# Kernel optimization log

Hardware: AMD Instinct MI355X
Metric: run time of the kernel (lower is better)

Reference implementation:

```python
import jax, jax.numpy as jnp
from jax import lax
import numpy as np

EPS = 1e-5

def _bn(x, g, b, m, v):
    # inference-mode BatchNorm2d over channel dim (NCHW)
    scale = (g * lax.rsqrt(v + EPS))[None, :, None, None]
    return (x - m[None, :, None, None]) * scale + b[None, :, None, None]

def _conv(x, w, dil, pad):
    return lax.conv_general_dilated(
        x, w, window_strides=(1, 1), padding=[(pad, pad), (pad, pad)],
        rhs_dilation=(dil, dil), dimension_numbers=('NCHW', 'OIHW', 'NCHW'))

def _interleave(b0, b1, b2, b3):
    # out[2i+r, 2j+c] = branch[2r+c][i, j]  (equivalent to the mask*nearest-upsample trick)
    bs, C, H, W = b0.shape
    row0 = jnp.stack([b0, b1], axis=-1)          # (bs,C,H,W,2) -> c
    row1 = jnp.stack([b2, b3], axis=-1)
    s = jnp.stack([row0, row1], axis=-2)          # (bs,C,H,W,2,2) -> (...,r,c)
    return s.transpose(0, 1, 2, 4, 3, 5).reshape(bs, C, 2 * H, 2 * W)

def setup_inputs() -> dict:
    key = jax.random.key(0)
    ks = iter(jax.random.split(key, 40))
    B, Cin, Cout, H = 8, 256, 128, 64
    inp = {"x": jax.random.normal(next(ks), (B, Cin, H, H), jnp.float32)}
    inp["w0"] = jax.random.normal(next(ks), (Cout, Cin, 1, 1), jnp.float32) * 0.05
    for i in (1, 2, 3):
        inp[f"w{i}"] = jax.random.normal(next(ks), (Cout, Cin, 3, 3), jnp.float32) * 0.02
    inp["wp"] = jax.random.normal(next(ks), (Cout, Cout, 1, 1), jnp.float32) * 0.05
    for t in ("0", "1", "2", "3", "p"):
        inp[f"g{t}"] = 1.0 + 0.1 * jax.random.normal(next(ks), (Cout,), jnp.float32)
        inp[f"b{t}"] = 0.1 * jax.random.normal(next(ks), (Cout,), jnp.float32)
        inp[f"m{t}"] = 0.05 * jax.random.normal(next(ks), (Cout,), jnp.float32)
        inp[f"v{t}"] = jax.random.uniform(next(ks), (Cout,), jnp.float32, 0.5, 1.5)
    return inp

def reference(x, w0, w1, w2, w3, wp,
              g0, b0, m0, v0, g1, b1, m1, v1,
              g2, b2, m2, v2, g3, b3, m3, v3,
              gp, bp, mp, vp):
    RATES = (6, 12, 18)
    br0 = jax.nn.relu(_bn(_conv(x, w0, 1, 0), g0, b0, m0, v0))
    br1 = jax.nn.relu(_bn(_conv(x, w1, RATES[0], RATES[0]), g1, b1, m1, v1))
    br2 = jax.nn.relu(_bn(_conv(x, w2, RATES[1], RATES[1]), g2, b2, m2, v2))
    br3 = jax.nn.relu(_bn(_conv(x, w3, RATES[2], RATES[2]), g3, b3, m3, v3))
    up = _interleave(br0, br1, br2, br3)          # (B, Cout, 2H, 2W)
    return jax.nn.relu(_bn(_conv(up, wp, 1, 0), gp, bp, mp, vp))  # dropout: eval identity
```

## Files before the change

### kernel.cpp

```cpp
#include <hip/hip_runtime.h>
#include <stdint.h>

typedef unsigned int uint32;
typedef uint16_t u16;
typedef short short8 __attribute__((ext_vector_type(8)));
typedef short shortx4 __attribute__((ext_vector_type(4)));
typedef float floatx4 __attribute__((ext_vector_type(4)));

#define BN_EPS 1e-5f

#define XROW 25600
#define XPLANE 1638400
#define XB_SHORTS 13107200
#define ZROW_SHORTS 25600

#define OFF0 0
#define OFF1 32768
#define OFF2 327680
#define OFF3 622592
#define OFFP 917504
#define WPK_SHORTS 933888
#define U_B0 4096
#define U_B  36864
#define U_TOT 116736

__device__ __forceinline__ u16 f2bf(float f) {
  uint32 u = __float_as_uint(f);
  u += 0x7fffu + ((u >> 16) & 1u);
  return (u16)(u >> 16);
}

__global__ void k_xcvt(const float* __restrict__ x, u16* __restrict__ xb) {
  int bid = blockIdx.x, tid = threadIdx.x;
  if (bid == 512) {
    uint32* z = (uint32*)(xb + XB_SHORTS);
    #pragma unroll
    for (int r = 0; r < 50; ++r) z[r * 256 + tid] = 0;
    return;
  }
  int n = bid >> 6, i = bid & 63;
  uint32* rw = (uint32*)(xb + (size_t)n * XPLANE + (size_t)i * XROW);
  #pragma unroll
  for (int e = 0; e < 18; ++e) {
    int idx = e * 256 + tid;
    int colid = idx >> 7;
    int jp = (colid < 18) ? colid : (colid + 64);
    rw[jp * 128 + (idx & 127)] = 0;
  }
  int ci2 = tid & 127, jh = tid >> 7;
  const float* xs = x + ((size_t)(n * 256 + 2 * ci2) * 64 + i) * 64 + jh * 32;
  #pragma unroll 4
  for (int j = 0; j < 32; ++j) {
    float f0 = xs[j];
    float f1 = xs[4096 + j];
    uint32 pk = (uint32)f2bf(f0) | ((uint32)f2bf(f1) << 16);
    rw[(jh * 32 + j + 18) * 128 + ci2] = pk;
  }
}

__global__ void k_wpack(const float* __restrict__ w0, const float* __restrict__ w1,
                        const float* __restrict__ w2, const float* __restrict__ w3,
                        const float* __restrict__ wp, u16* __restrict__ wpk) {
  int g = blockIdx.x * 256 + threadIdx.x;
  if (g >= U_TOT) return;
  const float* w; int Cin, t, q, u, off; bool k3;
  if (g < U_B0) {
    int blk = g >> 10; w = w0; Cin = 256; k3 = false; t = 0; q = blk; u = g & 1023;
    off = OFF0 + blk * 8192;
  } else if (g < U_B0 + U_B) {
    int g1 = g - U_B0; int blk = g1 >> 10; w = w1; Cin = 256; k3 = true;
    t = blk >> 2; q = blk & 3; u = g1 & 1023; off = OFF1 + blk * 8192;
  } else if (g < U_B0 + 2*U_B) {
    int g1 = g - (U_B0 + U_B); int blk = g1 >> 10; w = w2; Cin = 256; k3 = true;
    t = blk >> 2; q = blk & 3; u = g1 & 1023; off = OFF2 + blk * 8192;
  } else if (g < U_B0 + 3*U_B) {
    int g1 = g - (U_B0 + 2*U_B); int blk = g1 >> 10; w = w3; Cin = 256; k3 = true;
    t = blk >> 2; q = blk & 3; u = g1 & 1023; off = OFF3 + blk * 8192;
  } else {
    int g1 = g - (U_B0 + 3*U_B); int blk = g1 >> 10; w = wp; Cin = 128; k3 = false;
    t = 0; q = blk; u = g1 & 1023; off = OFFP + blk * 8192;
  }
  int slot = u >> 7, co = u & 127;
  int ci0 = q * 64 + slot * 8;
  int kh = k3 ? (t / 3) : 0, kw = k3 ? (t % 3) : 0;
  union { short8 s; u16 us[8]; } v;
  #pragma unroll
  for (int e = 0; e < 8; ++e) {
    int ci = ci0 + e;
    float wv = k3 ? w[((co * Cin + ci) * 3 + kh) * 3 + kw] : w[co * Cin + ci];
    v.us[e] = f2bf(wv);
  }
  *(short8*)(wpk + off + u * 8) = v.s;
}

__global__ void k_bn(const float* g0,const float* b0,const float* m0,const float* v0,
                     const float* g1,const float* b1,const float* m1,const float* v1,
                     const float* g2,const float* b2,const float* m2,const float* v2,
                     const float* g3,const float* b3,const float* m3,const float* v3,
                     const float* gp,const float* bp,const float* mp,const float* vp,
                     float* __restrict__ bn) {
  int i = blockIdx.x * 256 + threadIdx.x;
  if (i >= 640) return;
  int t = i >> 7, co = i & 127;
  const float *G, *B, *M, *V;
  if      (t == 0) { G=g0; B=b0; M=m0; V=v0; }
  else if (t == 1) { G=g1; B=b1; M=m1; V=v1; }
  else if (t == 2) { G=g2; B=b2; M=m2; V=v2; }
  else if (t == 3) { G=g3; B=b3; M=m3; V=v3; }
  else             { G=gp; B=bp; M=mp; V=vp; }
  float s = G[co] * rsqrtf(V[co] + BN_EPS);
  bn[t * 256 + co]       = s;
  bn[t * 256 + 128 + co] = B[co] - M[co] * s;
}

__global__ __launch_bounds__(256, 3)
void k_main(const u16* __restrict__ xb, const u16* __restrict__ wpk,
            const float* __restrict__ bn, float* __restrict__ out) {
  __shared__ __align__(16) u16 BP[16384];

  int tid = threadIdx.x;
  int bid = blockIdx.x;
  int n = bid & 7;
  int rest = bid >> 3;
  int tile = rest >> 2;
  int b = (rest ^ (rest >> 5)) & 3;
  int i0 = tile * 2;
  int lane = tid & 63, wid = tid >> 6;
  int wm = wid >> 1, wn = wid & 1;
  int m16 = lane & 15, hh = lane >> 4;

  const u16* xg = xb + (size_t)n * XPLANE;
  const u16* zr = xb + XB_SHORTS;
  int d = (b == 0) ? 0 : ((b == 1) ? 6 : ((b == 2) ? 12 : 18));
  int NS = ((b == 0) ? 1 : 9) * 4;
  int woff8 = ((b == 0) ? OFF0 : (b == 1) ? OFF1 : (b == 2) ? OFF2 : OFF3) / 8;

  const short8* wpk8 = (const short8*)wpk;
  const short8* PsS8 = (const short8*)BP;

  floatx4 acc[4][4];
  #pragma unroll
  for (int a1 = 0; a1 < 4; ++a1)
    #pragma unroll
    for (int a2 = 0; a2 < 4; ++a2) acc[a1][a2] = (floatx4){0.f, 0.f, 0.f, 0.f};

  short8 rb[4];
  int cg = tid & 7, pxo = tid >> 3;
  int arow = wm * 64 + m16;

  auto prefetchB = [&](int s) {
    int t = s >> 2, q = s & 3;
    int di = d * (t / 3 - 1);
    int dj = d * (t % 3 - 1);
    #pragma unroll
    for (int k = 0; k < 4; ++k) {
      int px = k * 32 + pxo;
      int ii = i0 + (k >> 1) + di;
      const u16* base = (ii >= 0 && ii < 64) ? (xg + ii * XROW) : zr;
      int jj = (px & 63) + 18 + dj;
      rb[k] = *(const short8*)(base + jj * 256 + q * 64 + cg * 8);
    }
  };

  prefetchB(0);

  for (int s = 0; s < NS; ++s) {
    short8* Bcur = (short8*)(BP + (s & 1) * 8192);
    #pragma unroll
    for (int k = 0; k < 4; ++k) {
      int px = k * 32 + pxo;
      Bcur[px * 8 + (cg ^ (px & 7))] = rb[k];
    }
    short8 af[2][4];
    {
      int abase = woff8 + s * 1024;
      #pragma unroll
      for (int kk = 0; kk < 2; ++kk)
        #pragma unroll
        for (int f = 0; f < 4; ++f)
          af[kk][f] = wpk8[abase + (kk * 4 + hh) * 128 + arow + f * 16];
    }
    if (s + 1 < NS) prefetchB(s + 1);
    asm volatile("s_waitcnt lgkmcnt(0)" ::: "memory");
    __builtin_amdgcn_s_barrier();
    __builtin_amdgcn_s_setprio(1);
    #pragma unroll
    for (int kk = 0; kk < 2; ++kk) {
      short8 bfr[4];
      #pragma unroll
      for (int f = 0; f < 4; ++f) {
        int px = wn * 64 + f * 16 + m16;
        bfr[f] = Bcur[px * 8 + ((kk * 4 + hh) ^ (px & 7))];
      }
      #pragma unroll
      for (int fm = 0; fm < 4; ++fm)
        #pragma unroll
        for (int fn = 0; fn < 4; ++fn)
          acc[fm][fn] = __builtin_amdgcn_mfma_f32_16x16x32_bf16(
              af[kk][fm], bfr[fn], acc[fm][fn], 0, 0, 0);
    }
    __builtin_amdgcn_s_setprio(0);
  }

  __syncthreads();
  #pragma unroll
  for (int fm = 0; fm < 4; ++fm) {
    int co_base = wm * 64 + fm * 16 + hh * 4;
    float sc[4], sh[4];
    #pragma unroll
    for (int r = 0; r < 4; ++r) {
      sc[r] = bn[b * 256 + co_base + r];
      sh[r] = bn[b * 256 + 128 + co_base + r];
    }
    #pragma unroll
    for (int fn = 0; fn < 4; ++fn) {
      int px = wn * 64 + fn * 16 + m16;
      int sw = (px >> 1) & 7;
      int slot = (co_base >> 3) ^ sw;
      union { shortx4 s4; u16 us[4]; } pk;
      #pragma unroll
      for (int r = 0; r < 4; ++r)
        pk.us[r] = f2bf(fmaxf(acc[fm][fn][r] * sc[r] + sh[r], 0.f));
      *(shortx4*)&BP[px * 128 + slot * 8 + (co_base & 7)] = pk.s4;
    }
  }

  floatx4 acc2[4][4];
  #pragma unroll
  for (int a1 = 0; a1 < 4; ++a1)
    #pragma unroll
    for (int a2 = 0; a2 < 4; ++a2) acc2[a1][a2] = (floatx4){0.f, 0.f, 0.f, 0.f};

  __syncthreads();
  #pragma unroll
  for (int q = 0; q < 2; ++q) {
    #pragma unroll
    for (int kk = 0; kk < 2; ++kk) {
      short8 af2[4], bfr[4];
      #pragma unroll
      for (int f = 0; f < 4; ++f)
        af2[f] = wpk8[OFFP / 8 + q * 1024 + (kk * 4 + hh) * 128 + arow + f * 16];
      #pragma unroll
      for (int f = 0; f < 4; ++f) {
        int px = wn * 64 + f * 16 + m16;
        int slot = q * 8 + kk * 4 + hh;
        bfr[f] = PsS8[px * 16 + (slot ^ ((px >> 1) & 7))];
      }
      #pragma unroll
      for (int fm = 0; fm < 4; ++fm)
        #pragma unroll
        for (int fn = 0; fn < 4; ++fn)
          acc2[fm][fn] = __builtin_amdgcn_mfma_f32_16x16x32_bf16(
              af2[fm], bfr[fn], acc2[fm][fn], 0, 0, 0);
    }
  }

  int rb2 = b >> 1, cb = b & 1;
  #pragma unroll
  for (int fm = 0; fm < 4; ++fm) {
    #pragma unroll
    for (int r = 0; r < 4; ++r) {
      int co = wm * 64 + fm * 16 + hh * 4 + r;
      float s  = bn[1024 + co];
      float sh = bn[1024 + 128 + co];
      #pragma unroll
      for (int fn = 0; fn < 4; ++fn) {
        int px = wn * 64 + fn * 16 + m16;
        int i = i0 + (px >> 6), j = px & 63;
        float v = fmaxf(acc2[fm][fn][r] * s + sh, 0.f);
        out[(((n * 128 + co) * 128) + (2 * i + rb2)) * 128 + (2 * j + cb)] = v;
      }
    }
  }
}

extern "C" void kernel_launch(void* const* d_in, const int* in_sizes, int n_in,
                              void* d_out, int out_size, void* d_ws, size_t ws_size,
                              hipStream_t stream) {
  const float* x  = (const float*)d_in[0];
  const float* w0 = (const float*)d_in[1];
  const float* w1 = (const float*)d_in[2];
  const float* w2 = (const float*)d_in[3];
  const float* w3 = (const float*)d_in[4];
  const float* wp = (const float*)d_in[5];

  u16* xbuf = (u16*)d_ws;
  u16* wpk  = (u16*)d_ws + (XB_SHORTS + ZROW_SHORTS);
  float* bn = (float*)((char*)d_ws + (size_t)(XB_SHORTS + ZROW_SHORTS + WPK_SHORTS) * 2);

  k_xcvt<<<513, 256, 0, stream>>>(x, xbuf);
  k_wpack<<<456, 256, 0, stream>>>(w0, w1, w2, w3, wp, wpk);
  k_bn<<<3, 256, 0, stream>>>(
      (const float*)d_in[6],  (const float*)d_in[7],  (const float*)d_in[8],  (const float*)d_in[9],
      (const float*)d_in[10], (const float*)d_in[11], (const float*)d_in[12], (const float*)d_in[13],
      (const float*)d_in[14], (const float*)d_in[15], (const float*)d_in[16], (const float*)d_in[17],
      (const float*)d_in[18], (const float*)d_in[19], (const float*)d_in[20], (const float*)d_in[21],
      (const float*)d_in[22], (const float*)d_in[23], (const float*)d_in[24], (const float*)d_in[25],
      bn);
  k_main<<<1024, 256, 0, stream>>>(xbuf, wpk, bn, (float*)d_out);
}
```

Before: 104.5 us.

## Stage input tiles with direct global-to-LDS loads and raise occupancy target

Replaces the register-staged prefetch of activation tiles (global load into registers, then ds_write) with global_load_lds, which writes directly into the double-buffered LDS tile. The XOR swizzle moves into the source address, and the next stage's load is issued after the barrier, with a vmcnt wait in place of the lgkm wait. It also raises launch bounds from 3 to 4 waves per SIMD and hoists the projection-weight loads ahead of the final syncthreads. This is meant to free VGPRs and cut LDS-write instructions to allow higher occupancy. The cost is a dependence on correct vmcnt accounting for the async LDS writes, plus possible spills under the tighter register budget.

```diff
diff --git a/kernel.cpp b/kernel.cpp
--- a/kernel.cpp
+++ b/kernel.cpp
@@ -113,7 +113,7 @@
   bn[t * 256 + 128 + co] = B[co] - M[co] * s;
 }
 
-__global__ __launch_bounds__(256, 3)
+__global__ __launch_bounds__(256, 4)
 void k_main(const u16* __restrict__ xb, const u16* __restrict__ wpk,
             const float* __restrict__ bn, float* __restrict__ out) {
   __shared__ __align__(16) u16 BP[16384];
@@ -137,6 +137,7 @@
 
   const short8* wpk8 = (const short8*)wpk;
   const short8* PsS8 = (const short8*)BP;
+  int arow = wm * 64 + m16;
 
   floatx4 acc[4][4];
   #pragma unroll
@@ -144,33 +145,30 @@
     #pragma unroll
     for (int a2 = 0; a2 < 4; ++a2) acc[a1][a2] = (floatx4){0.f, 0.f, 0.f, 0.f};
 
-  short8 rb[4];
-  int cg = tid & 7, pxo = tid >> 3;
-  int arow = wm * 64 + m16;
-
-  auto prefetchB = [&](int s) {
+  auto stageB = [&](int s) {
     int t = s >> 2, q = s & 3;
     int di = d * (t / 3 - 1);
     int dj = d * (t % 3 - 1);
+    u16* lb = BP + (s & 1) * 8192;
     #pragma unroll
     for (int k = 0; k < 4; ++k) {
-      int px = k * 32 + pxo;
-      int ii = i0 + (k >> 1) + di;
+      int pxblk = wid * 32 + k * 8;
+      int px = pxblk + (lane >> 3);
+      int ii = i0 + (pxblk >> 6) + di;
       const u16* base = (ii >= 0 && ii < 64) ? (xg + ii * XROW) : zr;
-      int jj = (px & 63) + 18 + dj;
-      rb[k] = *(const short8*)(base + jj * 256 + q * 64 + cg * 8);
+      int cg = (lane & 7) ^ (px & 7);
+      const u16* g = base + ((px & 63) + 18 + dj) * 256 + q * 64 + cg * 8;
+      __builtin_amdgcn_global_load_lds(
+          (const __attribute__((address_space(1))) void*)g,
+          (__attribute__((address_space(3))) void*)(lb + (wid * 4 + k) * 512),
+          16, 0, 0);
     }
   };
 
-  prefetchB(0);
+  stageB(0);
 
   for (int s = 0; s < NS; ++s) {
-    short8* Bcur = (short8*)(BP + (s & 1) * 8192);
-    #pragma unroll
-    for (int k = 0; k < 4; ++k) {
-      int px = k * 32 + pxo;
-      Bcur[px * 8 + (cg ^ (px & 7))] = rb[k];
-    }
+    const short8* Bcur = (const short8*)(BP + (s & 1) * 8192);
     short8 af[2][4];
     {
       int abase = woff8 + s * 1024;
@@ -180,9 +178,10 @@
         for (int f = 0; f < 4; ++f)
           af[kk][f] = wpk8[abase + (kk * 4 + hh) * 128 + arow + f * 16];
     }
-    if (s + 1 < NS) prefetchB(s + 1);
-    asm volatile("s_waitcnt lgkmcnt(0)" ::: "memory");
+    asm volatile("s_waitcnt vmcnt(4)" ::: "memory");
     __builtin_amdgcn_s_barrier();
+    __builtin_amdgcn_sched_barrier(0);
+    if (s + 1 < NS) stageB(s + 1);
     __builtin_amdgcn_s_setprio(1);
     #pragma unroll
     for (int kk = 0; kk < 2; ++kk) {
@@ -225,21 +224,28 @@
     }
   }
 
+  short8 af2[2][2][4];
+  #pragma unroll
+  for (int q = 0; q < 2; ++q)
+    #pragma unroll
+    for (int kk = 0; kk < 2; ++kk)
+      #pragma unroll
+      for (int f = 0; f < 4; ++f)
+        af2[q][kk][f] = wpk8[OFFP / 8 + q * 1024 + (kk * 4 + hh) * 128 + arow + f * 16];
+
+  __syncthreads();
+
   floatx4 acc2[4][4];
   #pragma unroll
   for (int a1 = 0; a1 < 4; ++a1)
     #pragma unroll
     for (int a2 = 0; a2 < 4; ++a2) acc2[a1][a2] = (floatx4){0.f, 0.f, 0.f, 0.f};
 
-  __syncthreads();
   #pragma unroll
   for (int q = 0; q < 2; ++q) {
     #pragma unroll
     for (int kk = 0; kk < 2; ++kk) {
-      short8 af2[4], bfr[4];
-      #pragma unroll
-      for (int f = 0; f < 4; ++f)
-        af2[f] = wpk8[OFFP / 8 + q * 1024 + (kk * 4 + hh) * 128 + arow + f * 16];
+      short8 bfr[4];
       #pragma unroll
       for (int f = 0; f < 4; ++f) {
         int px = wn * 64 + f * 16 + m16;
@@ -251,7 +257,7 @@
         #pragma unroll
         for (int fn = 0; fn < 4; ++fn)
           acc2[fm][fn] = __builtin_amdgcn_mfma_f32_16x16x32_bf16(
-              af2[fm], bfr[fn], acc2[fm][fn], 0, 0, 0);
+              af2[q][kk][fm], bfr[fn], acc2[fm][fn], 0, 0, 0);
     }
   }
 
```

Measured after the change: 106.1 us. About the same (+1.5%).
